# Optimization experiments

Measured on AMD Instinct MI355X. Metric: run time of the kernel, lower is better.

## Reference

```python
import jax, jax.numpy as jnp
import numpy as np
from jax import lax

B, H = 32768, 32  # batch, hidden_dim (hidden_dim=32 fixed by the source module)
T = 128           # num_steps


def setup_inputs() -> dict:
    key = jax.random.key(0)
    ks = jax.random.split(key, 8)
    s = 1.0 / np.sqrt(H)  # torch default uniform(-1/sqrt(H), 1/sqrt(H)) scale
    return {
        "in_data": jax.random.normal(ks[0], (B, H), dtype=jnp.float32),
        "hidden": jax.random.normal(ks[1], (B, H), dtype=jnp.float32),
        "W_ih": jax.random.uniform(ks[2], (3 * H, H), jnp.float32, -s, s),
        "W_hh": jax.random.uniform(ks[3], (3 * H, H), jnp.float32, -s, s),
        "b_ih": jax.random.uniform(ks[4], (3 * H,), jnp.float32, -s, s),
        "b_hh": jax.random.uniform(ks[5], (3 * H,), jnp.float32, -s, s),
        "W_out": jax.random.uniform(ks[6], (1, H), jnp.float32, -s, s),
        "b_out": jax.random.uniform(ks[7], (1,), jnp.float32, -s, s),
        "num_steps": T,
    }


def reference(in_data, hidden, W_ih, W_hh, b_ih, b_hh, W_out, b_out, num_steps):
    # the GRU hidden output is fed back as the next step's input.
    def gru_cell(x, h):
        gi = x @ W_ih.T + b_ih  # [B, 3H]
        gh = h @ W_hh.T + b_hh  # [B, 3H]
        i_r, i_z, i_n = jnp.split(gi, 3, axis=-1)
        h_r, h_z, h_n = jnp.split(gh, 3, axis=-1)
        r = jax.nn.sigmoid(i_r + h_r)
        z = jax.nn.sigmoid(i_z + h_z)
        n = jnp.tanh(i_n + r * h_n)
        return (1.0 - z) * n + z * h

    def step(carry, _):
        x, h = carry
        h_new = gru_cell(x, h)
        y = h_new @ W_out.T + b_out  # [B, 1]
        return (h_new, h_new), y[:, 0]

    _, ys = lax.scan(step, (in_data, hidden), None, length=num_steps)  # ys: [T, B]
    return ys.T  # [B, T], matching torch's stack().squeeze(2).permute(1,0)
```

## Files before the change

kernel.cpp:

```cpp
#include <hip/hip_runtime.h>


typedef __attribute__((ext_vector_type(8)))  short short8;
typedef __attribute__((ext_vector_type(4)))  float f32x4;

struct F3 { short8 h, m, l; };

__device__ __forceinline__ void ldrow8(const float* p, float f[8]) {
    f32x4 a = *(const f32x4*)p;
    f32x4 b = *(const f32x4*)(p + 4);
    f[0]=a[0]; f[1]=a[1]; f[2]=a[2]; f[3]=a[3];
    f[4]=b[0]; f[5]=b[1]; f[6]=b[2]; f[7]=b[3];
}
__device__ __forceinline__ void ldrow8s(const float* p, float f[8], float s) {
    ldrow8(p, f);
    #pragma unroll
    for (int i = 0; i < 8; ++i) f[i] *= s;
}

__device__ __forceinline__ F3 split8(const float f[8]) {
    unsigned H[8], M[8], L[8];
    #pragma unroll
    for (int i = 0; i < 8; ++i) {
        unsigned a = __float_as_uint(f[i]);
        unsigned h = a & 0xffff0000u;
        float    t = f[i] - __uint_as_float(h);
        unsigned m = __float_as_uint(t) & 0xffff0000u;
        float    u = t - __uint_as_float(m);
        unsigned l = __float_as_uint(u) & 0xffff0000u;
        H[i] = h; M[i] = m; L[i] = l;
    }
    union { unsigned u[4]; short8 s; } uh, um, ul;
    #pragma unroll
    for (int p = 0; p < 4; ++p) {
        uh.u[p] = __builtin_amdgcn_perm(H[2*p+1], H[2*p], 0x07060302u);
        um.u[p] = __builtin_amdgcn_perm(M[2*p+1], M[2*p], 0x07060302u);
        ul.u[p] = __builtin_amdgcn_perm(L[2*p+1], L[2*p], 0x07060302u);
    }
    F3 r; r.h = uh.s; r.m = um.s; r.l = ul.s; return r;
}

#define MFMA(a,b,c) __builtin_amdgcn_mfma_f32_16x16x32_bf16((a),(b),(c),0,0,0)

__device__ __forceinline__ f32x4 mm6(const F3& A, const F3& B, f32x4 c) {
    c = MFMA(A.h, B.l, c);
    c = MFMA(A.l, B.h, c);
    c = MFMA(A.m, B.m, c);
    c = MFMA(A.h, B.m, c);
    c = MFMA(A.m, B.h, c);
    c = MFMA(A.h, B.h, c);
    return c;
}

__device__ __forceinline__ void mfma8(const F3 A[8], const F3& Bv,
                                      const f32x4 bC[8], f32x4 C[8]) {
    #pragma unroll
    for (int rt = 0; rt < 8; ++rt) C[rt] = mm6(A[rt], Bv, bC[rt]);
}

__device__ __forceinline__ float rcp_nr(float x) {
    float r = __builtin_amdgcn_rcpf(x);
    return r * fmaf(-x, r, 2.f);
}
__device__ __forceinline__ float comb_(float arN, float azN, float anS, float ahnS, float hp) {
    float rr = rcp_nr(1.f + __builtin_amdgcn_exp2f(arN));
    float zz = rcp_nr(1.f + __builtin_amdgcn_exp2f(azN));
    float q  = rcp_nr(__builtin_amdgcn_exp2f(fmaf(rr, ahnS, anS)) + 1.f);
    float nn = fmaf(-2.f, q, 1.f);
    return fmaf(zz, hp - nn, nn);
}

__device__ __forceinline__ void combineG(const f32x4 C[8], float hp[8], F3& Bv,
                                         const float wl[4], const float wh[4],
                                         float boutv, float* op, int t, bool st) {
    float h8[8], yp = 0.f;
    #pragma unroll
    for (int r = 0; r < 4; ++r) {
        float a  = comb_(C[0][r], C[2][r], C[4][r], C[6][r], hp[r]);
        float b2 = comb_(C[1][r], C[3][r], C[5][r], C[7][r], hp[4 + r]);
        yp = fmaf(wl[r], a, yp);
        yp = fmaf(wh[r], b2, yp);
        h8[r] = a; h8[4 + r] = b2;
        hp[r] = a; hp[4 + r] = b2;
    }
    yp += __shfl_xor(yp, 16);
    yp += __shfl_xor(yp, 32);
    if (st) op[t] = yp + boutv;
    Bv = split8(h8);
}

__global__ __launch_bounds__(64, 1)
void gru_mfma(const float* __restrict__ in_data, const float* __restrict__ hidden,
              const float* __restrict__ W_ih,   const float* __restrict__ W_hh,
              const float* __restrict__ b_ih,   const float* __restrict__ b_hh,
              const float* __restrict__ W_out,  const float* __restrict__ b_out,
              float* __restrict__ out, int B, int T)
{
    const float S_RZ = -1.44269504088896340736f;
    const float S_N  =  2.88539008177792681472f;

    const int lane = threadIdx.x & 63;
    const int n    = lane & 15;
    const int g    = lane >> 4;
    const int k0   = g * 8;
    const long eA  = (long)blockIdx.x * 32 + n;
    const long eB  = eA + 16;

    const int rlo = 8 * (n >> 2) + (n & 3);
    const int rhi = rlo + 4;

    f32x4 bC[8];
    #pragma unroll
    for (int p = 0; p < 2; ++p) {
        #pragma unroll
        for (int r = 0; r < 4; ++r) {
            const int c = 8 * g + 4 * p + r;
            bC[0 + p][r] = S_RZ * (b_ih[c]      + b_hh[c]);
            bC[2 + p][r] = S_RZ * (b_ih[32 + c] + b_hh[32 + c]);
            bC[4 + p][r] = S_N  *  b_ih[64 + c];
            bC[6 + p][r] = S_N  *  b_hh[64 + c];
        }
    }
    float wl[4], wh[4];
    #pragma unroll
    for (int r = 0; r < 4; ++r) { wl[r] = W_out[8*g + r]; wh[r] = W_out[8*g + 4 + r]; }
    const float boutv = b_out[0];
    float* const opA = out + eA * (long)T;
    float* const opB = out + eB * (long)T;

    float hpA[8], hpB[8];
    F3 BvA, BvB, BxA, BxB;
    {
        float f[8];
        ldrow8(hidden + eA * 32 + k0, f);
        #pragma unroll
        for (int i = 0; i < 8; ++i) hpA[i] = f[i];
        BvA = split8(f);
        ldrow8(hidden + eB * 32 + k0, f);
        #pragma unroll
        for (int i = 0; i < 8; ++i) hpB[i] = f[i];
        BvB = split8(f);
        ldrow8(in_data + eA * 32 + k0, f); BxA = split8(f);
        ldrow8(in_data + eB * 32 + k0, f); BxB = split8(f);
    }

    F3 A[8];
    f32x4 CA[8], CB[8];

    #pragma unroll
    for (int gs = 0; gs < 3; ++gs) {
        const float s = (gs < 2) ? S_RZ : S_N;
        float fl[8], fh[8];
        ldrow8s(W_ih + (gs * 32 + rlo) * 32 + k0, fl, s);
        ldrow8s(W_ih + (gs * 32 + rhi) * 32 + k0, fh, s);
        A[2*gs] = split8(fl); A[2*gs+1] = split8(fh);
    }
    #pragma unroll
    for (int rt = 0; rt < 6; ++rt) { CA[rt] = mm6(A[rt], BxA, bC[rt]);
                                     CB[rt] = mm6(A[rt], BxB, bC[rt]); }

    #pragma unroll
    for (int gs = 0; gs < 3; ++gs) {
        const float s = (gs < 2) ? S_RZ : S_N;
        float fl[8], fh[8];
        ldrow8s(W_hh + (gs * 32 + rlo) * 32 + k0, fl, s);
        ldrow8s(W_hh + (gs * 32 + rhi) * 32 + k0, fh, s);
        A[2*gs] = split8(fl); A[2*gs+1] = split8(fh);
    }
    #pragma unroll
    for (int rt = 0; rt < 4; ++rt) { CA[rt] = mm6(A[rt], BvA, CA[rt]);
                                     CB[rt] = mm6(A[rt], BvB, CB[rt]); }
    CA[6] = mm6(A[4], BvA, bC[6]);  CB[6] = mm6(A[4], BvB, bC[6]);
    CA[7] = mm6(A[5], BvA, bC[7]);  CB[7] = mm6(A[5], BvB, bC[7]);

    #pragma unroll
    for (int gs = 0; gs < 2; ++gs) {
        float fl[8], fh[8], g2[8];
        ldrow8(W_ih + (gs * 32 + rlo) * 32 + k0, fl);
        ldrow8(W_hh + (gs * 32 + rlo) * 32 + k0, g2);
        #pragma unroll
        for (int i = 0; i < 8; ++i) fl[i] = S_RZ * (fl[i] + g2[i]);
        ldrow8(W_ih + (gs * 32 + rhi) * 32 + k0, fh);
        ldrow8(W_hh + (gs * 32 + rhi) * 32 + k0, g2);
        #pragma unroll
        for (int i = 0; i < 8; ++i) fh[i] = S_RZ * (fh[i] + g2[i]);
        A[2*gs] = split8(fl); A[2*gs+1] = split8(fh);
    }
    {
        float fl[8], fh[8];
        ldrow8s(W_ih + (64 + rlo) * 32 + k0, fl, S_N);
        ldrow8s(W_ih + (64 + rhi) * 32 + k0, fh, S_N);
        A[4] = split8(fl); A[5] = split8(fh);
        ldrow8s(W_hh + (64 + rlo) * 32 + k0, fl, S_N);
        ldrow8s(W_hh + (64 + rhi) * 32 + k0, fh, S_N);
        A[6] = split8(fl); A[7] = split8(fh);
    }

    const bool st = (lane < 16);

    combineG(CA, hpA, BvA, wl, wh, boutv, opA, 0, st);

    #pragma unroll 1
    for (int t = 0; t < T - 1; ++t) {
        mfma8(A, BvA, bC, CA);
        combineG(CB, hpB, BvB, wl, wh, boutv, opB, t, st);
        mfma8(A, BvB, bC, CB);
        combineG(CA, hpA, BvA, wl, wh, boutv, opA, t + 1, st);
    }

    combineG(CB, hpB, BvB, wl, wh, boutv, opB, T - 1, st);
}

extern "C" void kernel_launch(void* const* d_in, const int* in_sizes, int n_in,
                              void* d_out, int out_size, void* d_ws, size_t ws_size,
                              hipStream_t stream) {
    const float* in_data = (const float*)d_in[0];
    const float* hidden  = (const float*)d_in[1];
    const float* W_ih    = (const float*)d_in[2];
    const float* W_hh    = (const float*)d_in[3];
    const float* b_ih    = (const float*)d_in[4];
    const float* b_hh    = (const float*)d_in[5];
    const float* W_out   = (const float*)d_in[6];
    const float* b_out   = (const float*)d_in[7];
    float* out = (float*)d_out;

    const int B = in_sizes[0] / 32;
    const int T = out_size / B;
    const int blocks = B / 32;

    gru_mfma<<<blocks, 64, 0, stream>>>(in_data, hidden, W_ih, W_hh,
                                        b_ih, b_hh, W_out, b_out, out, B, T);
}
```

Baseline: 290.1 us.

## Split batch halves across two waves and compute output head with MFMA

Before, one wave carried two 16-row batch groups and interleaved their MFMA and gate phases by hand. Now each block runs two waves, one group per wave, so the hardware interleaves the waves instead. The scalar output projection moves from per-lane FMAs plus cross-lane shuffles to an extra split-bf16 MFMA against W_out with b_out as the accumulator seed. Waves raise their priority during the MFMA phase, and odd wave slots sleep once at start to stagger the two waves. The per-step critical path gets shorter, at the cost of six more MFMAs per step, redundant stores from lanes sharing a column, and reliance on the scheduler overlapping the two waves.

```diff
diff --git a/kernel.cpp b/kernel.cpp
--- a/kernel.cpp
+++ b/kernel.cpp
@@ -52,12 +52,6 @@
     return c;
 }
 
-__device__ __forceinline__ void mfma8(const F3 A[8], const F3& Bv,
-                                      const f32x4 bC[8], f32x4 C[8]) {
-    #pragma unroll
-    for (int rt = 0; rt < 8; ++rt) C[rt] = mm6(A[rt], Bv, bC[rt]);
-}
-
 __device__ __forceinline__ float rcp_nr(float x) {
     float r = __builtin_amdgcn_rcpf(x);
     return r * fmaf(-x, r, 2.f);
@@ -70,26 +64,19 @@
     return fmaf(zz, hp - nn, nn);
 }
 
-__device__ __forceinline__ void combineG(const f32x4 C[8], float hp[8], F3& Bv,
-                                         const float wl[4], const float wh[4],
-                                         float boutv, float* op, int t, bool st) {
-    float h8[8], yp = 0.f;
+__device__ __forceinline__ void combineG(const f32x4 C[8], float hp[8], F3& Bv) {
+    float h8[8];
     #pragma unroll
     for (int r = 0; r < 4; ++r) {
         float a  = comb_(C[0][r], C[2][r], C[4][r], C[6][r], hp[r]);
         float b2 = comb_(C[1][r], C[3][r], C[5][r], C[7][r], hp[4 + r]);
-        yp = fmaf(wl[r], a, yp);
-        yp = fmaf(wh[r], b2, yp);
         h8[r] = a; h8[4 + r] = b2;
         hp[r] = a; hp[4 + r] = b2;
     }
-    yp += __shfl_xor(yp, 16);
-    yp += __shfl_xor(yp, 32);
-    if (st) op[t] = yp + boutv;
     Bv = split8(h8);
 }
 
-__global__ __launch_bounds__(64, 1)
+__global__ __launch_bounds__(128, 2)
 void gru_mfma(const float* __restrict__ in_data, const float* __restrict__ hidden,
               const float* __restrict__ W_ih,   const float* __restrict__ W_hh,
               const float* __restrict__ b_ih,   const float* __restrict__ b_hh,
@@ -99,12 +86,13 @@
     const float S_RZ = -1.44269504088896340736f;
     const float S_N  =  2.88539008177792681472f;
 
-    const int lane = threadIdx.x & 63;
+    const int tid  = threadIdx.x;
+    const int lane = tid & 63;
+    const int wv   = tid >> 6;
     const int n    = lane & 15;
     const int g    = lane >> 4;
     const int k0   = g * 8;
-    const long eA  = (long)blockIdx.x * 32 + n;
-    const long eB  = eA + 16;
+    const long e   = (long)blockIdx.x * 32 + wv * 16 + n;
 
     const int rlo = 8 * (n >> 2) + (n & 3);
     const int rhi = rlo + 4;
@@ -121,31 +109,25 @@
             bC[6 + p][r] = S_N  *  b_hh[64 + c];
         }
     }
-    float wl[4], wh[4];
-    #pragma unroll
-    for (int r = 0; r < 4; ++r) { wl[r] = W_out[8*g + r]; wh[r] = W_out[8*g + 4 + r]; }
-    const float boutv = b_out[0];
-    float* const opA = out + eA * (long)T;
-    float* const opB = out + eB * (long)T;
-
-    float hpA[8], hpB[8];
-    F3 BvA, BvB, BxA, BxB;
+    f32x4 bC8;
+    { float bo = b_out[0]; bC8[0]=bo; bC8[1]=bo; bC8[2]=bo; bC8[3]=bo; }
+    float* const op = out + e * (long)T;
+
+    float hp[8];
+    F3 Bv, Bx;
     {
         float f[8];
-        ldrow8(hidden + eA * 32 + k0, f);
-        #pragma unroll
-        for (int i = 0; i < 8; ++i) hpA[i] = f[i];
-        BvA = split8(f);
-        ldrow8(hidden + eB * 32 + k0, f);
-        #pragma unroll
-        for (int i = 0; i < 8; ++i) hpB[i] = f[i];
-        BvB = split8(f);
-        ldrow8(in_data + eA * 32 + k0, f); BxA = split8(f);
-        ldrow8(in_data + eB * 32 + k0, f); BxB = split8(f);
-    }
-
-    F3 A[8];
-    f32x4 CA[8], CB[8];
+        ldrow8(hidden + e * 32 + k0, f);
+        #pragma unroll
+        for (int i = 0; i < 8; ++i) hp[i] = f[i];
+        Bv = split8(f);
+        ldrow8(in_data + e * 32 + k0, f); Bx = split8(f);
+    }
+
+    F3 A[8], Ay;
+    f32x4 C[8], Cy;
+
+    { float f[8]; ldrow8(W_out + k0, f); Ay = split8(f); }
 
     #pragma unroll
     for (int gs = 0; gs < 3; ++gs) {
@@ -156,8 +138,7 @@
         A[2*gs] = split8(fl); A[2*gs+1] = split8(fh);
     }
     #pragma unroll
-    for (int rt = 0; rt < 6; ++rt) { CA[rt] = mm6(A[rt], BxA, bC[rt]);
-                                     CB[rt] = mm6(A[rt], BxB, bC[rt]); }
+    for (int rt = 0; rt < 6; ++rt) C[rt] = mm6(A[rt], Bx, bC[rt]);
 
     #pragma unroll
     for (int gs = 0; gs < 3; ++gs) {
@@ -168,10 +149,9 @@
         A[2*gs] = split8(fl); A[2*gs+1] = split8(fh);
     }
     #pragma unroll
-    for (int rt = 0; rt < 4; ++rt) { CA[rt] = mm6(A[rt], BvA, CA[rt]);
-                                     CB[rt] = mm6(A[rt], BvB, CB[rt]); }
-    CA[6] = mm6(A[4], BvA, bC[6]);  CB[6] = mm6(A[4], BvB, bC[6]);
-    CA[7] = mm6(A[5], BvA, bC[7]);  CB[7] = mm6(A[5], BvB, bC[7]);
+    for (int rt = 0; rt < 4; ++rt) C[rt] = mm6(A[rt], Bv, C[rt]);
+    C[6] = mm6(A[4], Bv, bC[6]);
+    C[7] = mm6(A[5], Bv, bC[7]);
 
     #pragma unroll
     for (int gs = 0; gs < 2; ++gs) {
@@ -196,19 +176,26 @@
         A[6] = split8(fl); A[7] = split8(fh);
     }
 
-    const bool st = (lane < 16);
-
-    combineG(CA, hpA, BvA, wl, wh, boutv, opA, 0, st);
+    combineG(C, hp, Bv);
+
+    {
+        int wslot = __builtin_amdgcn_s_getreg((3 << 11) | (0 << 6) | 4);
+        if (wslot & 1) __builtin_amdgcn_s_sleep(18);
+    }
 
     #pragma unroll 1
     for (int t = 0; t < T - 1; ++t) {
-        mfma8(A, BvA, bC, CA);
-        combineG(CB, hpB, BvB, wl, wh, boutv, opB, t, st);
-        mfma8(A, BvB, bC, CB);
-        combineG(CA, hpA, BvA, wl, wh, boutv, opA, t + 1, st);
-    }
-
-    combineG(CB, hpB, BvB, wl, wh, boutv, opB, T - 1, st);
+        __builtin_amdgcn_s_setprio(1);
+        #pragma unroll
+        for (int rt = 0; rt < 8; ++rt) C[rt] = mm6(A[rt], Bv, bC[rt]);
+        Cy = mm6(Ay, Bv, bC8);
+        __builtin_amdgcn_s_setprio(0);
+        combineG(C, hp, Bv);
+        op[t] = Cy[0];
+    }
+
+    Cy = mm6(Ay, Bv, bC8);
+    op[T - 1] = Cy[0];
 }
 
 extern "C" void kernel_launch(void* const* d_in, const int* in_sizes, int n_in,
@@ -228,6 +215,6 @@
     const int T = out_size / B;
     const int blocks = B / 32;
 
-    gru_mfma<<<blocks, 64, 0, stream>>>(in_data, hidden, W_ih, W_hh,
-                                        b_ih, b_hh, W_out, b_out, out, B, T);
-}
+    gru_mfma<<<blocks, 128, 0, stream>>>(in_data, hidden, W_ih, W_hh,
+                                         b_ih, b_hh, W_out, b_out, out, B, T);
+}
```

New measurement: 277.5 us. 4.4% less time.
